# Performance work log

Hardware: AMD Instinct MI355X
Metric: run time of the kernel (lower is better)

The kernel has to match this reference:

```python
import jax, jax.numpy as jnp
import numpy as np

B, H, W = 1, 48, 160
CIN, CF, D = 1024, 64, 48  # input_features, PSM_features, depth_channel = max_disp/downsample
EPS = 1e-5


def setup_inputs() -> dict:
    key = jax.random.key(0)
    ks = jax.random.split(key, 12)
    z = lambda s: jnp.zeros(s, jnp.float32)
    o = lambda s: jnp.ones(s, jnp.float32)
    return {
        "left_features": jax.random.normal(ks[0], (B, CIN, H, W), jnp.float32),
        "right_features": jax.random.normal(ks[1], (B, CIN, H, W), jnp.float32),
        "conv1_w": jax.random.normal(ks[2], (CF, CIN), jnp.float32) * 0.03,
        "conv1_b": z((CF,)),
        "bn1_g": o((CF,)), "bn1_b": z((CF,)),
        "bn1_m": jax.random.normal(ks[3], (CF,), jnp.float32) * 0.1,
        "bn1_v": jax.random.uniform(ks[4], (CF,), jnp.float32) + 0.5,
        "c3a_w": jax.random.normal(ks[5], (CF, 2 * CF, 3, 3, 3), jnp.float32) * 0.02,
        "c3a_b": z((CF,)),
        "bn3a_g": o((CF,)), "bn3a_b": z((CF,)),
        "bn3a_m": jax.random.normal(ks[6], (CF,), jnp.float32) * 0.1,
        "bn3a_v": jax.random.uniform(ks[7], (CF,), jnp.float32) + 0.5,
        "c3b_w": jax.random.normal(ks[8], (CF, CF, 3, 3, 3), jnp.float32) * 0.02,
        "c3b_b": z((CF,)),
        "bn3b_g": o((CF,)), "bn3b_b": z((CF,)),
        "bn3b_m": jax.random.normal(ks[9], (CF,), jnp.float32) * 0.1,
        "bn3b_v": jax.random.uniform(ks[10], (CF,), jnp.float32) + 0.5,
    }


def _bn(x, g, b, m, v, nsp):
    # eval-mode batchnorm; nsp = number of trailing spatial dims
    sh = (-1,) + (1,) * nsp
    return (x - m.reshape(sh)) * (g.reshape(sh) * jax.lax.rsqrt(v.reshape(sh) + EPS)) + b.reshape(sh)


def reference(left_features, right_features, conv1_w, conv1_b, bn1_g, bn1_b, bn1_m, bn1_v,
              c3a_w, c3a_b, bn3a_g, bn3a_b, bn3a_m, bn3a_v,
              c3b_w, c3b_b, bn3b_g, bn3b_b, bn3b_m, bn3b_v):
    def down(x):
        y = jnp.einsum('oi,bihw->bohw', conv1_w, x) + conv1_b[:, None, None]
        return jax.nn.relu(_bn(y, bn1_g, bn1_b, bn1_m, bn1_v, 2))

    L = down(left_features)   # [B,CF,H,W]
    R = down(right_features)  # [B,CF,H,W]

    # Vectorized shifted cost volume (replaces the Python loop over disparities).
    # For disparity d, output width j: left -> L[...,j] if j>=d else 0; right -> R[...,j-d] if j>=d else 0.
    idx = jnp.arange(W)[None, :] - jnp.arange(D)[:, None]       # [D,W]
    mask = (idx >= 0).astype(L.dtype)                           # [D,W]
    left_vol = L[:, :, :, None, :] * mask                       # [B,CF,H,D,W]
    right_vol = R[:, :, :, jnp.clip(idx, 0, W - 1)] * mask      # [B,CF,H,D,W]
    cost = jnp.concatenate([left_vol, right_vol], axis=1)       # [B,2CF,H,D,W]
    cost = jnp.transpose(cost, (0, 1, 3, 2, 4))                 # [B,2CF,D,H,W]

    def conv3(x, wk, bias):
        y = jax.lax.conv_general_dilated(x, wk, (1, 1, 1), [(1, 1)] * 3,
                                         dimension_numbers=('NCDHW', 'OIDHW', 'NCDHW'))
        return y + bias[:, None, None, None]

    y = jax.nn.relu(_bn(conv3(cost, c3a_w, c3a_b), bn3a_g, bn3a_b, bn3a_m, bn3a_v, 3))
    y = jax.nn.relu(_bn(conv3(y, c3b_w, c3b_b), bn3b_g, bn3b_b, bn3b_m, bn3b_v, 3))
    return y.reshape(B, -1, H, W)  # [B, CF*D, H, W]
```

## Files before the change

kernel.cpp:

```cpp
#include <hip/hip_runtime.h>
#include <hip/hip_bf16.h>


#define HH   48
#define WW   160
#define DDEP 48
#define CIN  1024
#define NPX  (HH*WW)
#define KSPL 8

typedef unsigned short u16;
typedef unsigned int   u32;
typedef __attribute__((ext_vector_type(8))) short bf16x8;
typedef __attribute__((ext_vector_type(4))) float f32x4;
typedef __attribute__((ext_vector_type(4))) u32   u32x4;
typedef __attribute__((ext_vector_type(2))) u32   u32x2;

__device__ __forceinline__ u16 f2bf(float f) {
    u32 u = __builtin_bit_cast(u32, f);
    u32 r = u + 0x7FFFu + ((u >> 16) & 1u);
    return (u16)(r >> 16);
}

__global__ __launch_bounds__(256) void k_prep(
    const float* __restrict__ c3a, const float* __restrict__ c3b,
    const float* __restrict__ cb3a, const float* __restrict__ g3a,
    const float* __restrict__ b3a,  const float* __restrict__ m3a,
    const float* __restrict__ v3a,
    const float* __restrict__ cb3b, const float* __restrict__ g3b,
    const float* __restrict__ b3b,  const float* __restrict__ m3b,
    const float* __restrict__ v3b,
    u16* __restrict__ wa, u16* __restrict__ wb, float* __restrict__ bnc)
{
    int tid = blockIdx.x*256 + threadIdx.x;
    if (tid < 221184) {
        int i = tid & 127, o = (tid >> 7) & 63, tap = tid >> 13;
        wa[tid] = f2bf(c3a[(o*128 + i)*27 + tap]);
    } else {
        int t2 = tid - 221184;
        if (t2 < 110592) {
            int i = t2 & 63;
            int kw = (t2 >> 6) % 3;
            int rest = t2 / 192;
            int o = rest & 63, kdkh = rest >> 6;
            wb[t2] = f2bf(c3b[(o*64 + i)*27 + (kdkh/3)*9 + (kdkh%3)*3 + kw]);
        }
    }
    if (tid < 64) {
        float s = g3a[tid] * rsqrtf(v3a[tid] + 1e-5f);
        bnc[tid]      = s;
        bnc[64 + tid] = (cb3a[tid] - m3a[tid])*s + b3a[tid];
    } else if (tid < 128) {
        int o = tid - 64;
        float s = g3b[o] * rsqrtf(v3b[o] + 1e-5f);
        bnc[128 + o] = s;
        bnc[192 + o] = (cb3b[o] - m3b[o])*s + b3b[o];
    }
}

__global__ __launch_bounds__(256) void k_conv1(
    const float* __restrict__ left, const float* __restrict__ right,
    const float* __restrict__ w1, float* __restrict__ P)
{
    __shared__ float Ws[8192];
    const int img = blockIdx.y;
    const int s   = blockIdx.z;
    const float* x = img ? right : left;
    const int tid = threadIdx.x;
    const int px = blockIdx.x*64 + (tid & 63);
    const int o0 = (tid >> 6)*16;
    const int ibase = s*(CIN/KSPL);

    #pragma unroll
    for (int q = 0; q < 8; ++q) {
        int idx = q*256 + tid;
        int o = idx >> 5, ii = (idx & 31)*4;
        *(f32x4*)(Ws + o*128 + ii) =
            *(const f32x4*)(w1 + (size_t)o*CIN + ibase + ii);
    }
    __syncthreads();

    float acc[16];
    #pragma unroll
    for (int oo = 0; oo < 16; ++oo) acc[oo] = 0.f;

    for (int it = 0; it < CIN/KSPL; it += 4) {
        const int i = ibase + it;
        float x0 = x[(i+0)*NPX + px];
        float x1 = x[(i+1)*NPX + px];
        float x2 = x[(i+2)*NPX + px];
        float x3 = x[(i+3)*NPX + px];
        #pragma unroll
        for (int oo = 0; oo < 16; ++oo) {
            const float4 wv4 = *(const float4*)(Ws + (o0+oo)*128 + it);
            acc[oo] = fmaf(wv4.w, x3, fmaf(wv4.z, x2,
                      fmaf(wv4.y, x1, fmaf(wv4.x, x0, acc[oo]))));
        }
    }
    float* dst = P + ((size_t)(s*2 + img)*NPX + px)*64 + o0;
    #pragma unroll
    for (int q = 0; q < 4; ++q)
        *(f32x4*)(dst + q*4) = *(const f32x4*)(acc + q*4);
}

__global__ __launch_bounds__(256) void k_conv1_reduce(
    const float* __restrict__ P,
    const float* __restrict__ b1,
    const float* __restrict__ g,  const float* __restrict__ bb,
    const float* __restrict__ m,  const float* __restrict__ v,
    u16* __restrict__ LRb)
{
    const int tid = blockIdx.x*256 + threadIdx.x;
    const int f = tid*4;
    f32x4 acc = *(const f32x4*)(P + f);
    #pragma unroll
    for (int s = 1; s < KSPL; ++s)
        acc += *(const f32x4*)(P + (size_t)(s*2)*(NPX*64) + f);
    const int o0 = f & 63;
    const int px = f >> 6;
    const int img = px / NPX, pxl = px - img*NPX;
    const int h = pxl / WW, w = pxl - h*WW;
    u16 res[4];
    #pragma unroll
    for (int r = 0; r < 4; ++r) {
        int o = o0 + r;
        float sc = g[o] * rsqrtf(v[o] + 1e-5f);
        float val = (acc[r] + b1[o] - m[o])*sc + bb[o];
        res[r] = f2bf(val > 0.f ? val : 0.f);
    }
    u16* dst = LRb + (size_t)img*491520 + h*10240 + (o0 >> 3)*1280
                   + w*8 + (o0 & 7);
    *(u32x2*)dst = *(const u32x2*)res;
}

__global__ __launch_bounds__(256) void k_conv3a(
    const u16* __restrict__ LRb, const u16* __restrict__ wa,
    const float* __restrict__ bnc, u16* __restrict__ yt)
{
    __shared__ u16 Aw[26112];

    const int h  = blockIdx.x;
    const int d0 = blockIdx.y*2;
    const int tid = threadIdx.x;
    const int l  = tid & 63;
    const int wv = tid >> 6;
    const int dd = wv >> 1;
    const int wbase = (wv & 1)*80;
    const int l15 = l & 15, l4 = l >> 4;
    const int wcol = wbase + l15;
    const bf16x8 bzero = {0,0,0,0,0,0,0,0};

    f32x4 acc[4][5];
    #pragma unroll
    for (int a = 0; a < 4; ++a)
        #pragma unroll
        for (int b = 0; b < 5; ++b)
            acc[a][b] = (f32x4){0.f,0.f,0.f,0.f};

    for (int kh = 0; kh < 3; ++kh) {
        int hp = h + kh - 1;
        if (hp < 0 || hp >= HH) continue;
        const u16* lrow = LRb + (size_t)hp*10240;
        const u16* rrow = LRb + 491520 + (size_t)hp*10240;
        for (int kd = 0; kd < 3; ++kd) {
            __syncthreads();
            {
                const u16* as = wa + (size_t)(kd*9 + kh*3)*8192;
                #pragma unroll
                for (int q = 0; q < 12; ++q) {
                    int idx = q*256 + tid;
                    int t = idx >> 10;
                    int e = idx & 1023;
                    int o = e >> 4, ii = (e & 15)*8;
                    *(u32x4*)(Aw + t*8704 + o*136 + ii) =
                        *(const u32x4*)(as + (size_t)idx*8);
                }
            }
            __syncthreads();

            const int dp = d0 + dd + kd - 1;
            const bool dok = (dp >= 0) && (dp < DDEP);
            for (int kw = 0; kw < 3; ++kw) {
                const u16* awk = Aw + kw*8704;
                int lofs[5], rofs[5];
                bool val[5];
                #pragma unroll
                for (int nf = 0; nf < 5; ++nf) {
                    int wp = wcol + nf*16 + kw - 1;
                    bool vv = dok && (wp >= 0) && (wp < WW) && (wp >= dp);
                    val[nf]  = vv;
                    lofs[nf] = (vv ? wp : 0)*8;
                    rofs[nf] = (vv ? (wp - dp) : 0)*8;
                }
                #pragma unroll
                for (int ic = 0; ic < 4; ++ic) {
                    const int kcolA = ic*32 + 8*l4;
                    bf16x8 a0 = *(const bf16x8*)(awk + ( 0 + l15)*136 + kcolA);
                    bf16x8 a1 = *(const bf16x8*)(awk + (16 + l15)*136 + kcolA);
                    bf16x8 a2 = *(const bf16x8*)(awk + (32 + l15)*136 + kcolA);
                    bf16x8 a3 = *(const bf16x8*)(awk + (48 + l15)*136 + kcolA);
                    const u16* bbase = ((ic < 2) ? lrow : rrow)
                                     + (size_t)((ic & 1)*4 + l4)*1280;
                    #pragma unroll
                    for (int nf = 0; nf < 5; ++nf) {
                        bf16x8 b = *(const bf16x8*)(bbase +
                                       ((ic < 2) ? lofs[nf] : rofs[nf]));
                        b = val[nf] ? b : bzero;
                        acc[0][nf] = __builtin_amdgcn_mfma_f32_16x16x32_bf16(a0, b, acc[0][nf], 0, 0, 0);
                        acc[1][nf] = __builtin_amdgcn_mfma_f32_16x16x32_bf16(a1, b, acc[1][nf], 0, 0, 0);
                        acc[2][nf] = __builtin_amdgcn_mfma_f32_16x16x32_bf16(a2, b, acc[2][nf], 0, 0, 0);
                        acc[3][nf] = __builtin_amdgcn_mfma_f32_16x16x32_bf16(a3, b, acc[3][nf], 0, 0, 0);
                    }
                }
            }
        }
    }

    float sc[4][4], sh[4][4];
    #pragma unroll
    for (int mf = 0; mf < 4; ++mf)
        #pragma unroll
        for (int r = 0; r < 4; ++r) {
            int o = mf*16 + 4*l4 + r;
            sc[mf][r] = bnc[o];
            sh[mf][r] = bnc[64 + o];
        }
    const int dy = d0 + dd;
    u16* rowb = yt + (size_t)(dy*HH + h)*10240;
    #pragma unroll
    for (int mf = 0; mf < 4; ++mf)
        #pragma unroll
        for (int nf = 0; nf < 5; ++nf) {
            const int w = wbase + nf*16 + l15;
            #pragma unroll
            for (int rp = 0; rp < 2; ++rp) {
                int o_lo = mf*16 + 4*l4 + rp*2;
                float v0 = acc[mf][nf][rp*2]  *sc[mf][rp*2]   + sh[mf][rp*2];
                float v1 = acc[mf][nf][rp*2+1]*sc[mf][rp*2+1] + sh[mf][rp*2+1];
                v0 = v0 > 0.f ? v0 : 0.f;
                v1 = v1 > 0.f ? v1 : 0.f;
                u32 pk = (u32)f2bf(v0) | ((u32)f2bf(v1) << 16);
                *(u32*)(rowb + (o_lo >> 3)*1280 + w*8 + (o_lo & 7)) = pk;
            }
        }
}

__global__ __launch_bounds__(256) void k_conv3b(
    const u16* __restrict__ yt, const u16* __restrict__ wb,
    const float* __restrict__ bnc, float* __restrict__ outp)
{
    __shared__ u16 A2[12800];

    const int h  = blockIdx.x;
    const int d0 = blockIdx.y*2;
    const int tid = threadIdx.x;
    const int l  = tid & 63;
    const int wv = tid >> 6;
    const int dd = wv >> 1;
    const int wbase = (wv & 1)*80;
    const int l15 = l & 15, l4 = l >> 4;
    const int wcol = wbase + l15;
    const bf16x8 bzero = {0,0,0,0,0,0,0,0};

    f32x4 acc[4][5];
    #pragma unroll
    for (int a = 0; a < 4; ++a)
        #pragma unroll
        for (int b = 0; b < 5; ++b)
            acc[a][b] = (f32x4){0.f,0.f,0.f,0.f};

    for (int kh = 0; kh < 3; ++kh) {
        int hp = h + kh - 1;
        if (hp < 0 || hp >= HH) continue;
        for (int kd = 0; kd < 3; ++kd) {
            __syncthreads();
            {
                const u16* as = wb + (size_t)(kd*3 + kh)*12288;
                #pragma unroll
                for (int q = 0; q < 6; ++q) {
                    int idx = q*256 + tid;
                    int o = idx/24;
                    int cc = (idx - o*24)*8;
                    *(u32x4*)(A2 + o*200 + cc) = *(const u32x4*)(as + (size_t)idx*8);
                }
            }
            __syncthreads();

            const int dpw = d0 + dd + kd - 1;
            const bool dok = (dpw >= 0) && (dpw < DDEP);
            const int dc = min(max(dpw, 0), DDEP-1);
            const u16* yrow = yt + ((size_t)((dc*HH + hp)*8) + l4)*1280;
            for (int kw = 0; kw < 3; ++kw) {
                int gofs[5]; bool val[5];
                #pragma unroll
                for (int nf = 0; nf < 5; ++nf) {
                    int wp = wcol + nf*16 + kw - 1;
                    bool vv = dok && (wp >= 0) && (wp < WW);
                    val[nf]  = vv;
                    gofs[nf] = (vv ? wp : 0)*8;
                }
                #pragma unroll
                for (int ic = 0; ic < 2; ++ic) {
                    const int kcolA = kw*64 + ic*32 + 8*l4;
                    bf16x8 a0 = *(const bf16x8*)(A2 + ( 0 + l15)*200 + kcolA);
                    bf16x8 a1 = *(const bf16x8*)(A2 + (16 + l15)*200 + kcolA);
                    bf16x8 a2 = *(const bf16x8*)(A2 + (32 + l15)*200 + kcolA);
                    bf16x8 a3 = *(const bf16x8*)(A2 + (48 + l15)*200 + kcolA);
                    const u16* yc = yrow + ic*5120;
                    #pragma unroll
                    for (int nf = 0; nf < 5; ++nf) {
                        bf16x8 b = *(const bf16x8*)(yc + gofs[nf]);
                        b = val[nf] ? b : bzero;
                        acc[0][nf] = __builtin_amdgcn_mfma_f32_16x16x32_bf16(a0, b, acc[0][nf], 0, 0, 0);
                        acc[1][nf] = __builtin_amdgcn_mfma_f32_16x16x32_bf16(a1, b, acc[1][nf], 0, 0, 0);
                        acc[2][nf] = __builtin_amdgcn_mfma_f32_16x16x32_bf16(a2, b, acc[2][nf], 0, 0, 0);
                        acc[3][nf] = __builtin_amdgcn_mfma_f32_16x16x32_bf16(a3, b, acc[3][nf], 0, 0, 0);
                    }
                }
            }
        }
    }

    const int dout = d0 + dd;
    #pragma unroll
    for (int mf = 0; mf < 4; ++mf)
        #pragma unroll
        for (int r = 0; r < 4; ++r) {
            int o = mf*16 + 4*l4 + r;
            float s = bnc[128 + o], t = bnc[192 + o];
            size_t base = ((size_t)(o*DDEP + dout)*HH + h)*WW + wbase;
            #pragma unroll
            for (int nf = 0; nf < 5; ++nf) {
                float vv = acc[mf][nf][r]*s + t;
                outp[base + nf*16 + l15] = vv > 0.f ? vv : 0.f;
            }
        }
}

extern "C" void kernel_launch(void* const* d_in, const int* in_sizes, int n_in,
                              void* d_out, int out_size, void* d_ws, size_t ws_size,
                              hipStream_t stream)
{
    const float* left  = (const float*)d_in[0];
    const float* right = (const float*)d_in[1];
    const float* w1    = (const float*)d_in[2];
    const float* b1    = (const float*)d_in[3];
    const float* g1    = (const float*)d_in[4];
    const float* bb1   = (const float*)d_in[5];
    const float* m1    = (const float*)d_in[6];
    const float* v1    = (const float*)d_in[7];
    const float* c3a   = (const float*)d_in[8];
    const float* cb3a  = (const float*)d_in[9];
    const float* g3a   = (const float*)d_in[10];
    const float* b3a   = (const float*)d_in[11];
    const float* m3a   = (const float*)d_in[12];
    const float* v3a   = (const float*)d_in[13];
    const float* c3b   = (const float*)d_in[14];
    const float* cb3b  = (const float*)d_in[15];
    const float* g3b   = (const float*)d_in[16];
    const float* b3b   = (const float*)d_in[17];
    const float* m3b   = (const float*)d_in[18];
    const float* v3b   = (const float*)d_in[19];

    char* ws = (char*)d_ws;
    u16*   LRb = (u16*)ws;
    u16*   wa  = (u16*)(ws + 1966080);
    u16*   wb  = (u16*)(ws + 1966080 + 442368);
    float* bnc = (float*)(ws + 1966080 + 442368 + 221184);
    u16*   yt  = (u16*)(ws + 1966080 + 442368 + 221184 + 1024);
    if (ws_size < 49816576) return;

    float* P = (float*)d_out;

    k_prep<<<dim3(1296), dim3(256), 0, stream>>>(
        c3a, c3b, cb3a, g3a, b3a, m3a, v3a, cb3b, g3b, b3b, m3b, v3b, wa, wb, bnc);
    k_conv1<<<dim3(120, 2, KSPL), dim3(256), 0, stream>>>(
        left, right, w1, P);
    k_conv1_reduce<<<dim3(960), dim3(256), 0, stream>>>(
        P, b1, g1, bb1, m1, v1, LRb);
    k_conv3a<<<dim3(48, 24), dim3(256), 0, stream>>>(LRb, wa, bnc, yt);
    k_conv3b<<<dim3(48, 24), dim3(256), 0, stream>>>(yt, wb, bnc, (float*)d_out);
}
```

Baseline: 367.9 us.

## Software-pipeline conv3a B-operand loads and double conv1 K-split

The conv3a inner loop is restructured so global loads of the B fragments for the next two (kw, ic) groups are issued ahead of the MFMAs that consume the current group, using two register buffers. The first two loads also overlap with the shared-memory weight staging and its barriers. Launch bounds now request 3 waves per SIMD to limit register growth. Separately, conv1's K-split rises from 8 to 16, halving per-block shared weights and doubling the grid, at the cost of more partial sums for the reduce kernel to read.

```diff
diff --git a/kernel.cpp b/kernel.cpp
--- a/kernel.cpp
+++ b/kernel.cpp
@@ -7,7 +7,7 @@
 #define DDEP 48
 #define CIN  1024
 #define NPX  (HH*WW)
-#define KSPL 8
+#define KSPL 16
 
 typedef unsigned short u16;
 typedef unsigned int   u32;
@@ -62,7 +62,7 @@
     const float* __restrict__ left, const float* __restrict__ right,
     const float* __restrict__ w1, float* __restrict__ P)
 {
-    __shared__ float Ws[8192];
+    __shared__ float Ws[4096];
     const int img = blockIdx.y;
     const int s   = blockIdx.z;
     const float* x = img ? right : left;
@@ -72,10 +72,10 @@
     const int ibase = s*(CIN/KSPL);
 
     #pragma unroll
-    for (int q = 0; q < 8; ++q) {
+    for (int q = 0; q < 4; ++q) {
         int idx = q*256 + tid;
-        int o = idx >> 5, ii = (idx & 31)*4;
-        *(f32x4*)(Ws + o*128 + ii) =
+        int o = idx >> 4, ii = (idx & 15)*4;
+        *(f32x4*)(Ws + o*64 + ii) =
             *(const f32x4*)(w1 + (size_t)o*CIN + ibase + ii);
     }
     __syncthreads();
@@ -92,7 +92,7 @@
         float x3 = x[(i+3)*NPX + px];
         #pragma unroll
         for (int oo = 0; oo < 16; ++oo) {
-            const float4 wv4 = *(const float4*)(Ws + (o0+oo)*128 + it);
+            const float4 wv4 = *(const float4*)(Ws + (o0+oo)*64 + it);
             acc[oo] = fmaf(wv4.w, x3, fmaf(wv4.z, x2,
                       fmaf(wv4.y, x1, fmaf(wv4.x, x0, acc[oo]))));
         }
@@ -133,7 +133,47 @@
     *(u32x2*)dst = *(const u32x2*)res;
 }
 
-__global__ __launch_bounds__(256) void k_conv3a(
+__device__ __forceinline__ void cv3a_issue(
+    bf16x8 (&Pb)[5], int g, int dp, bool dok, int wcol, int l4,
+    const u16* __restrict__ lrow, const u16* __restrict__ rrow)
+{
+    const int kw = g >> 2, ic = g & 3;
+    const u16* base = ((ic < 2) ? lrow : rrow)
+                    + (size_t)((ic & 1)*4 + l4)*1280;
+    #pragma unroll
+    for (int nf = 0; nf < 5; ++nf) {
+        int wp = wcol + nf*16 + kw - 1;
+        bool vv = dok && (wp >= 0) && (wp < WW) && (wp >= dp);
+        int ofs = (vv ? ((ic < 2) ? wp : (wp - dp)) : 0)*8;
+        Pb[nf] = *(const bf16x8*)(base + ofs);
+    }
+}
+
+__device__ __forceinline__ void cv3a_consume(
+    f32x4 (&acc)[4][5], const bf16x8 (&Pb)[5], const u16* __restrict__ Aw,
+    int g, int dp, bool dok, int wcol, int l4, int l15)
+{
+    const int kw = g >> 2, ic = g & 3;
+    const bf16x8 bzero = {0,0,0,0,0,0,0,0};
+    const u16* awk = Aw + kw*8704;
+    const int kcolA = ic*32 + 8*l4;
+    bf16x8 a0 = *(const bf16x8*)(awk + ( 0 + l15)*136 + kcolA);
+    bf16x8 a1 = *(const bf16x8*)(awk + (16 + l15)*136 + kcolA);
+    bf16x8 a2 = *(const bf16x8*)(awk + (32 + l15)*136 + kcolA);
+    bf16x8 a3 = *(const bf16x8*)(awk + (48 + l15)*136 + kcolA);
+    #pragma unroll
+    for (int nf = 0; nf < 5; ++nf) {
+        int wp = wcol + nf*16 + kw - 1;
+        bool vv = dok && (wp >= 0) && (wp < WW) && (wp >= dp);
+        bf16x8 b = vv ? Pb[nf] : bzero;
+        acc[0][nf] = __builtin_amdgcn_mfma_f32_16x16x32_bf16(a0, b, acc[0][nf], 0, 0, 0);
+        acc[1][nf] = __builtin_amdgcn_mfma_f32_16x16x32_bf16(a1, b, acc[1][nf], 0, 0, 0);
+        acc[2][nf] = __builtin_amdgcn_mfma_f32_16x16x32_bf16(a2, b, acc[2][nf], 0, 0, 0);
+        acc[3][nf] = __builtin_amdgcn_mfma_f32_16x16x32_bf16(a3, b, acc[3][nf], 0, 0, 0);
+    }
+}
+
+__global__ __launch_bounds__(256, 3) void k_conv3a(
     const u16* __restrict__ LRb, const u16* __restrict__ wa,
     const float* __restrict__ bnc, u16* __restrict__ yt)
 {
@@ -148,7 +188,6 @@
     const int wbase = (wv & 1)*80;
     const int l15 = l & 15, l4 = l >> 4;
     const int wcol = wbase + l15;
-    const bf16x8 bzero = {0,0,0,0,0,0,0,0};
 
     f32x4 acc[4][5];
     #pragma unroll
@@ -163,6 +202,13 @@
         const u16* lrow = LRb + (size_t)hp*10240;
         const u16* rrow = LRb + 491520 + (size_t)hp*10240;
         for (int kd = 0; kd < 3; ++kd) {
+            const int dp = d0 + dd + kd - 1;
+            const bool dok = (dp >= 0) && (dp < DDEP);
+
+            bf16x8 P0[5], P1[5];
+            cv3a_issue(P0, 0, dp, dok, wcol, l4, lrow, rrow);
+            cv3a_issue(P1, 1, dp, dok, wcol, l4, lrow, rrow);
+
             __syncthreads();
             {
                 const u16* as = wa + (size_t)(kd*9 + kh*3)*8192;
@@ -178,39 +224,16 @@
             }
             __syncthreads();
 
-            const int dp = d0 + dd + kd - 1;
-            const bool dok = (dp >= 0) && (dp < DDEP);
-            for (int kw = 0; kw < 3; ++kw) {
-                const u16* awk = Aw + kw*8704;
-                int lofs[5], rofs[5];
-                bool val[5];
-                #pragma unroll
-                for (int nf = 0; nf < 5; ++nf) {
-                    int wp = wcol + nf*16 + kw - 1;
-                    bool vv = dok && (wp >= 0) && (wp < WW) && (wp >= dp);
-                    val[nf]  = vv;
-                    lofs[nf] = (vv ? wp : 0)*8;
-                    rofs[nf] = (vv ? (wp - dp) : 0)*8;
-                }
-                #pragma unroll
-                for (int ic = 0; ic < 4; ++ic) {
-                    const int kcolA = ic*32 + 8*l4;
-                    bf16x8 a0 = *(const bf16x8*)(awk + ( 0 + l15)*136 + kcolA);
-                    bf16x8 a1 = *(const bf16x8*)(awk + (16 + l15)*136 + kcolA);
-                    bf16x8 a2 = *(const bf16x8*)(awk + (32 + l15)*136 + kcolA);
-                    bf16x8 a3 = *(const bf16x8*)(awk + (48 + l15)*136 + kcolA);
-                    const u16* bbase = ((ic < 2) ? lrow : rrow)
-                                     + (size_t)((ic & 1)*4 + l4)*1280;
-                    #pragma unroll
-                    for (int nf = 0; nf < 5; ++nf) {
-                        bf16x8 b = *(const bf16x8*)(bbase +
-                                       ((ic < 2) ? lofs[nf] : rofs[nf]));
-                        b = val[nf] ? b : bzero;
-                        acc[0][nf] = __builtin_amdgcn_mfma_f32_16x16x32_bf16(a0, b, acc[0][nf], 0, 0, 0);
-                        acc[1][nf] = __builtin_amdgcn_mfma_f32_16x16x32_bf16(a1, b, acc[1][nf], 0, 0, 0);
-                        acc[2][nf] = __builtin_amdgcn_mfma_f32_16x16x32_bf16(a2, b, acc[2][nf], 0, 0, 0);
-                        acc[3][nf] = __builtin_amdgcn_mfma_f32_16x16x32_bf16(a3, b, acc[3][nf], 0, 0, 0);
-                    }
+            #pragma unroll
+            for (int g = 0; g < 12; ++g) {
+                if ((g & 1) == 0) {
+                    cv3a_consume(acc, P0, Aw, g, dp, dok, wcol, l4, l15);
+                    if (g + 2 < 12)
+                        cv3a_issue(P0, g + 2, dp, dok, wcol, l4, lrow, rrow);
+                } else {
+                    cv3a_consume(acc, P1, Aw, g, dp, dok, wcol, l4, l15);
+                    if (g + 2 < 12)
+                        cv3a_issue(P1, g + 2, dp, dok, wcol, l4, lrow, rrow);
                 }
             }
         }
```

New measurement: 391.5 us. +6.4%, slower.
